# Kernel tuning notes

Measured on AMD Instinct MI355X. Metric: run time of the kernel, lower is better.

The kernel has to match this reference:

```python
import jax, jax.numpy as jnp
import numpy as np

N_NODES, N_EDGES, NNZ, F_IN, HID, K = 50000, 10000, 800000, 128, 512, 10


def setup_inputs() -> dict:
    key = jax.random.key(0)
    ks = jax.random.split(key, 6)
    x = jax.random.normal(ks[0], (N_NODES, F_IN), dtype=jnp.float32)
    node_idx = jax.random.randint(ks[1], (NNZ,), 0, N_NODES)
    edge_idx = jax.random.randint(ks[2], (NNZ,), 0, N_EDGES)
    hyperedge_index = jnp.stack([node_idx, edge_idx]).astype(jnp.int64)
    edge_weight = jax.random.uniform(ks[3], (N_EDGES,), dtype=jnp.float32, minval=0.5, maxval=1.5)
    theta = jax.random.normal(ks[4], (K + 1,), dtype=jnp.float32) * 0.1
    lin1_w = jax.random.normal(ks[5], (HID, F_IN), dtype=jnp.float32) * (1.0 / np.sqrt(F_IN))
    lin1_b = jnp.zeros((HID,), dtype=jnp.float32)
    return {"x": x, "hyperedge_index": hyperedge_index, "edge_weight": edge_weight,
            "theta": theta, "lin1_w": lin1_w, "lin1_b": lin1_b}


def _hyper_prop_factory(node_idx, edge_idx, edge_weight, n_nodes, n_edges):
    """Returns A_norm @ x where A_norm = Dv^-1/2 H W De^-1 H^T Dv^-1/2."""
    ones = jnp.ones_like(node_idx, dtype=edge_weight.dtype)
    d_e = jax.ops.segment_sum(ones, edge_idx, num_segments=n_edges)            # edge degree
    d_v = jax.ops.segment_sum(edge_weight[edge_idx], node_idx, num_segments=n_nodes)
    dv_is = jnp.where(d_v > 0, jax.lax.rsqrt(jnp.maximum(d_v, 1e-12)), 0.0)
    de_w = edge_weight * jnp.where(d_e > 0, 1.0 / jnp.maximum(d_e, 1e-12), 0.0)

    def prop(x):
        xv = x * dv_is[:, None]                                               # [N, F]
        m_e = jax.ops.segment_sum(xv[node_idx], edge_idx, num_segments=n_edges)
        m_e = m_e * de_w[:, None]                                             # [E, F]
        out = jax.ops.segment_sum(m_e[edge_idx], node_idx, num_segments=n_nodes)
        return out * dv_is[:, None]

    return prop


def cheb_hypergraph(x, node_idx, edge_idx, edge_weight, theta, n_nodes, n_edges):
    # L_tilde = L - I = -A_norm (lambda_max = 2). Chebyshev recurrence on L_tilde.
    prop = _hyper_prop_factory(node_idx, edge_idx, edge_weight, n_nodes, n_edges)
    t_prev = x                       # T_0
    out = theta[0] * t_prev
    t_cur = -prop(x)                 # T_1 = L_tilde x
    out = out + theta[1] * t_cur
    for k in range(2, theta.shape[0]):
        t_next = -2.0 * prop(t_cur) - t_prev   # T_k = 2 L_tilde T_{k-1} - T_{k-2}
        out = out + theta[k] * t_next
        t_prev, t_cur = t_cur, t_next
    return out


def reference(x, hyperedge_index, edge_weight, theta, lin1_w, lin1_b):
    node_idx = hyperedge_index[0]
    edge_idx = hyperedge_index[1]
    n_nodes = x.shape[0]
    n_edges = edge_weight.shape[0]
    # eval mode: both dropouts are identity
    h = cheb_hypergraph(x, node_idx, edge_idx, edge_weight, theta, n_nodes, n_edges)
    h = jnp.einsum('nf,hf->nh', h, lin1_w) + lin1_b
    # is_bns=False -> no batch norm; act_fn='relu'
    return jax.nn.relu(h)
```

## Files before the change

kernel.cpp:

```cpp
#include <hip/hip_runtime.h>


#define N_NODES 50000
#define N_EDGES 10000
#define NNZ     800000
#define F_IN    128
#define HID     512
#define F4      (F_IN / 4)
#define R16     16
#define NB_E    10
#define NB_N    49
#define HB      64
#define NW_E    (N_EDGES / 2)
#define NW_N    (N_NODES / 2)

typedef __attribute__((ext_vector_type(8))) short bf16x8;
typedef __attribute__((ext_vector_type(4))) float f32x4;

static __device__ __forceinline__ unsigned short f2bf(float f) {
    union { float f; unsigned u; } c; c.f = f;
    unsigned u = c.u;
    unsigned r = (u + 0x7fffu + ((u >> 16) & 1u)) >> 16;
    return (unsigned short)r;
}
static __device__ __forceinline__ float blo(unsigned u) {
    union { unsigned u; float f; } c; c.u = u << 16; return c.f;
}
static __device__ __forceinline__ float bhi(unsigned u) {
    union { unsigned u; float f; } c; c.u = u & 0xffff0000u; return c.f;
}
static __device__ __forceinline__ unsigned pack2(float lo, float hi) {
    return (unsigned)f2bf(lo) | ((unsigned)f2bf(hi) << 16);
}

__global__ __launch_bounds__(1024) void k_hist(const int* __restrict__ hidx,
                                               unsigned short* __restrict__ loc_e,
                                               unsigned short* __restrict__ loc_v,
                                               unsigned* __restrict__ hist_e,
                                               unsigned* __restrict__ hist_n) {
    __shared__ unsigned she[NW_E];
    __shared__ unsigned shn[NW_N];
    int tid = (int)threadIdx.x;
    for (int w = tid; w < NW_E; w += 1024) she[w] = 0;
    for (int w = tid; w < NW_N; w += 1024) shn[w] = 0;
    __syncthreads();
    int bid = (int)blockIdx.x;
    for (int i = bid * 1024 + tid; i < NNZ; i += HB * 1024) {
        int v = hidx[i];
        int e = hidx[NNZ + i];
        v = min(max(v, 0), N_NODES - 1);
        e = min(max(e, 0), N_EDGES - 1);
        int se = (e & 1) * 16;
        int sv = (v & 1) * 16;
        unsigned oe = atomicAdd(&she[e >> 1], 1u << se);
        unsigned ov = atomicAdd(&shn[v >> 1], 1u << sv);
        loc_e[i] = (unsigned short)((oe >> se) & 0xFFFFu);
        loc_v[i] = (unsigned short)((ov >> sv) & 0xFFFFu);
    }
    __syncthreads();
    for (int w = tid; w < NW_E; w += 1024) hist_e[bid * NW_E + w] = she[w];
    for (int w = tid; w < NW_N; w += 1024) hist_n[bid * NW_N + w] = shn[w];
}

__global__ void k_combine(const unsigned* __restrict__ hist_e,
                          const unsigned* __restrict__ hist_n,
                          int* __restrict__ base_e,
                          int* __restrict__ base_n,
                          int* __restrict__ counts_e,
                          int* __restrict__ counts_n) {
    int i = blockIdx.x * blockDim.x + threadIdx.x;
    if (i < N_EDGES) {
        int sh = (i & 1) * 16;
        int w = i >> 1;
        int s = 0;
#pragma unroll 8
        for (int b = 0; b < HB; ++b) {
            base_e[b * N_EDGES + i] = s;
            s += (int)((hist_e[b * NW_E + w] >> sh) & 0xFFFFu);
        }
        counts_e[i] = s;
    }
    if (i < N_NODES) {
        int sh = (i & 1) * 16;
        int w = i >> 1;
        int s = 0;
#pragma unroll 8
        for (int b = 0; b < HB; ++b) {
            base_n[b * N_NODES + i] = s;
            s += (int)((hist_n[b * NW_N + w] >> sh) & 0xFFFFu);
        }
        counts_n[i] = s;
    }
}

__global__ __launch_bounds__(1024) void k_scan_blk2(const int* __restrict__ ce,
                                                    const int* __restrict__ cn,
                                                    int* __restrict__ oute,
                                                    int* __restrict__ outn,
                                                    int* __restrict__ pe,
                                                    int* __restrict__ pn) {
    __shared__ int sd[1024];
    int b = (int)blockIdx.x;
    const int* counts; int n; int* out; int* partial; int lb;
    if (b < NB_E) { counts = ce; n = N_EDGES; out = oute; partial = pe; lb = b; }
    else          { counts = cn; n = N_NODES; out = outn; partial = pn; lb = b - NB_E; }
    int tid = (int)threadIdx.x;
    int i = lb * 1024 + tid;
    int v = (i < n) ? counts[i] : 0;
    sd[tid] = v;
    __syncthreads();
    for (int off = 1; off < 1024; off <<= 1) {
        int t = (tid >= off) ? sd[tid - off] : 0;
        __syncthreads();
        sd[tid] += t;
        __syncthreads();
    }
    if (i < n) out[i] = sd[tid] - v;
    if (tid == 1023) partial[lb] = sd[1023];
}

__global__ void k_scan_top2(int* __restrict__ pe, int* __restrict__ pn,
                            int* __restrict__ tot_e, int* __restrict__ tot_n) {
    int w = (int)threadIdx.x >> 6;
    int lane = (int)threadIdx.x & 63;
    int* partial = w ? pn : pe;
    int nb       = w ? NB_N : NB_E;
    int* total   = w ? tot_n : tot_e;
    int v = (lane < nb) ? partial[lane] : 0;
    int incl = v;
    for (int off = 1; off < 64; off <<= 1) {
        int t = __shfl_up(incl, off);
        if (lane >= off) incl += t;
    }
    if (lane < nb) partial[lane] = incl - v;
    if (lane == 63) *total = incl;
}

__global__ __launch_bounds__(1024) void k_scan_add2(int* __restrict__ oute,
                                                    int* __restrict__ outn,
                                                    const int* __restrict__ pe,
                                                    const int* __restrict__ pn) {
    int b = (int)blockIdx.x;
    int* out; const int* partial; int n; int lb;
    if (b < NB_E) { out = oute; partial = pe; n = N_EDGES; lb = b; }
    else          { out = outn; partial = pn; n = N_NODES; lb = b - NB_E; }
    int i = lb * 1024 + (int)threadIdx.x;
    if (i < n) out[i] += partial[lb];
}

__global__ void k_fill(const int* __restrict__ hidx,
                       const int* __restrict__ edge_ptr,
                       const int* __restrict__ node_ptr,
                       const unsigned short* __restrict__ loc_e,
                       const unsigned short* __restrict__ loc_v,
                       const int* __restrict__ base_e,
                       const int* __restrict__ base_n,
                       int* __restrict__ edge_node,
                       int* __restrict__ node_edge) {
    int i = blockIdx.x * blockDim.x + threadIdx.x;
    if (i >= NNZ) return;
    int wg = (i >> 10) & (HB - 1);
    int v = hidx[i];
    int e = hidx[NNZ + i];
    v = min(max(v, 0), N_NODES - 1);
    e = min(max(e, 0), N_EDGES - 1);
    edge_node[edge_ptr[e] + base_e[wg * N_EDGES + e] + (int)loc_e[i]] = v;
    node_edge[node_ptr[v] + base_n[wg * N_NODES + v] + (int)loc_v[i]] = e;
}

__global__ void k_norms2(const float* __restrict__ ew,
                         const int* __restrict__ edge_ptr,
                         const int* __restrict__ node_ptr,
                         const int* __restrict__ node_edge,
                         float* __restrict__ dv_is,
                         float* __restrict__ de_w) {
    int i = blockIdx.x * blockDim.x + threadIdx.x;
    if (i < N_NODES) {
        int s = node_ptr[i], t = node_ptr[i + 1];
        float d = 0.f;
        for (int j = s; j < t; ++j) d += ew[node_edge[j]];
        dv_is[i] = (d > 0.f) ? rsqrtf(fmaxf(d, 1e-12f)) : 0.f;
    }
    if (i < N_EDGES) {
        int c = edge_ptr[i + 1] - edge_ptr[i];
        de_w[i] = ew[i] * ((c > 0) ? (1.f / (float)c) : 0.f);
    }
}

__global__ void k_init(const float* __restrict__ x,
                       const float* __restrict__ theta,
                       const float* __restrict__ dv_is,
                       uint4* __restrict__ bufA,
                       float* __restrict__ acc) {
    int i = blockIdx.x * blockDim.x + threadIdx.x;
    if (i >= N_NODES * R16) return;
    int v = i >> 4;
    float dvv = dv_is[v];
    float w = (dvv > 0.f) ? dvv : 1.f;
    float4 x0 = ((const float4*)x)[2 * i];
    float4 x1 = ((const float4*)x)[2 * i + 1];
    uint4 q;
    q.x = pack2(w * x0.x, w * x0.y); q.y = pack2(w * x0.z, w * x0.w);
    q.z = pack2(w * x1.x, w * x1.y); q.w = pack2(w * x1.z, w * x1.w);
    bufA[i] = q;
    float t0 = theta[0];
    float4 a0, a1;
    a0.x = t0 * x0.x; a0.y = t0 * x0.y; a0.z = t0 * x0.z; a0.w = t0 * x0.w;
    a1.x = t0 * x1.x; a1.y = t0 * x1.y; a1.z = t0 * x1.z; a1.w = t0 * x1.w;
    ((float4*)acc)[2 * i]     = a0;
    ((float4*)acc)[2 * i + 1] = a1;
}

__global__ void k_phaseA(const uint4* __restrict__ tin,
                         const float* __restrict__ de_w,
                         const int* __restrict__ edge_ptr,
                         const int* __restrict__ edge_node,
                         uint4* __restrict__ m_e) {
    int tid    = (int)threadIdx.x;
    int g      = tid >> 6;
    int l64    = tid & 63;
    int stream = l64 >> 4;
    int lane   = l64 & 15;
    int e = blockIdx.x * 4 + g;
    int s = edge_ptr[e], t = edge_ptr[e + 1];
    float a0=0.f,a1=0.f,a2=0.f,a3=0.f,a4=0.f,a5=0.f,a6=0.f,a7=0.f;
    int j = s + stream;
    for (; j + 12 < t; j += 16) {
        int v0 = edge_node[j];
        int v1 = edge_node[j + 4];
        int v2 = edge_node[j + 8];
        int v3 = edge_node[j + 12];
        uint4 q0 = tin[v0 * R16 + lane];
        uint4 q1 = tin[v1 * R16 + lane];
        uint4 q2 = tin[v2 * R16 + lane];
        uint4 q3 = tin[v3 * R16 + lane];
        a0 += (blo(q0.x) + blo(q1.x)) + (blo(q2.x) + blo(q3.x));
        a1 += (bhi(q0.x) + bhi(q1.x)) + (bhi(q2.x) + bhi(q3.x));
        a2 += (blo(q0.y) + blo(q1.y)) + (blo(q2.y) + blo(q3.y));
        a3 += (bhi(q0.y) + bhi(q1.y)) + (bhi(q2.y) + bhi(q3.y));
        a4 += (blo(q0.z) + blo(q1.z)) + (blo(q2.z) + blo(q3.z));
        a5 += (bhi(q0.z) + bhi(q1.z)) + (bhi(q2.z) + bhi(q3.z));
        a6 += (blo(q0.w) + blo(q1.w)) + (blo(q2.w) + blo(q3.w));
        a7 += (bhi(q0.w) + bhi(q1.w)) + (bhi(q2.w) + bhi(q3.w));
    }
    for (; j < t; j += 4) {
        int v0 = edge_node[j];
        uint4 q0 = tin[v0 * R16 + lane];
        a0 += blo(q0.x); a1 += bhi(q0.x);
        a2 += blo(q0.y); a3 += bhi(q0.y);
        a4 += blo(q0.z); a5 += bhi(q0.z);
        a6 += blo(q0.w); a7 += bhi(q0.w);
    }
    a0 += __shfl_xor(a0, 16); a1 += __shfl_xor(a1, 16);
    a2 += __shfl_xor(a2, 16); a3 += __shfl_xor(a3, 16);
    a4 += __shfl_xor(a4, 16); a5 += __shfl_xor(a5, 16);
    a6 += __shfl_xor(a6, 16); a7 += __shfl_xor(a7, 16);
    a0 += __shfl_xor(a0, 32); a1 += __shfl_xor(a1, 32);
    a2 += __shfl_xor(a2, 32); a3 += __shfl_xor(a3, 32);
    a4 += __shfl_xor(a4, 32); a5 += __shfl_xor(a5, 32);
    a6 += __shfl_xor(a6, 32); a7 += __shfl_xor(a7, 32);
    if (stream == 0) {
        float w = de_w[e];
        uint4 o;
        o.x = pack2(a0 * w, a1 * w); o.y = pack2(a2 * w, a3 * w);
        o.z = pack2(a4 * w, a5 * w); o.w = pack2(a6 * w, a7 * w);
        m_e[e * R16 + lane] = o;
    }
}

__global__ void k_phaseB(const uint4* __restrict__ m_e,
                         const uint4* __restrict__ tin,
                         const float* __restrict__ dv_is,
                         const int* __restrict__ node_ptr,
                         const int* __restrict__ node_edge,
                         uint4* __restrict__ tio,
                         float* __restrict__ acc,
                         const float* __restrict__ theta, int k,
                         float ca, float cb, int accMode) {
    int g      = threadIdx.x >> 5;
    int stream = (threadIdx.x >> 4) & 1;
    int lane   = threadIdx.x & 15;
    int v = blockIdx.x * 8 + g;
    int s = node_ptr[v], t = node_ptr[v + 1];
    float s0=0.f,s1=0.f,s2=0.f,s3=0.f,s4=0.f,s5=0.f,s6=0.f,s7=0.f;
    int j = s + stream;
    for (; j + 2 < t; j += 4) {
        int e0 = node_edge[j];
        int e1 = node_edge[j + 2];
        uint4 q0 = m_e[e0 * R16 + lane];
        uint4 q1 = m_e[e1 * R16 + lane];
        s0 += blo(q0.x) + blo(q1.x); s1 += bhi(q0.x) + bhi(q1.x);
        s2 += blo(q0.y) + blo(q1.y); s3 += bhi(q0.y) + bhi(q1.y);
        s4 += blo(q0.z) + blo(q1.z); s5 += bhi(q0.z) + bhi(q1.z);
        s6 += blo(q0.w) + blo(q1.w); s7 += bhi(q0.w) + bhi(q1.w);
    }
    if (j < t) {
        int e0 = node_edge[j];
        uint4 q0 = m_e[e0 * R16 + lane];
        s0 += blo(q0.x); s1 += bhi(q0.x);
        s2 += blo(q0.y); s3 += bhi(q0.y);
        s4 += blo(q0.z); s5 += bhi(q0.z);
        s6 += blo(q0.w); s7 += bhi(q0.w);
    }
    s0 += __shfl_xor(s0, 16); s1 += __shfl_xor(s1, 16);
    s2 += __shfl_xor(s2, 16); s3 += __shfl_xor(s3, 16);
    s4 += __shfl_xor(s4, 16); s5 += __shfl_xor(s5, 16);
    s6 += __shfl_xor(s6, 16); s7 += __shfl_xor(s7, 16);
    if (stream == 0) {
        float dvv = dv_is[v];
        float scf = ca * dvv * dvv;
        int idx = v * R16 + lane;
        uint4 tp = tio[idx];
        float t0 = scf * s0 + cb * blo(tp.x);
        float t1 = scf * s1 + cb * bhi(tp.x);
        float t2 = scf * s2 + cb * blo(tp.y);
        float t3 = scf * s3 + cb * bhi(tp.y);
        float t4 = scf * s4 + cb * blo(tp.z);
        float t5 = scf * s5 + cb * bhi(tp.z);
        float t6 = scf * s6 + cb * blo(tp.w);
        float t7 = scf * s7 + cb * bhi(tp.w);
        uint4 tn;
        tn.x = pack2(t0, t1); tn.y = pack2(t2, t3);
        tn.z = pack2(t4, t5); tn.w = pack2(t6, t7);
        tio[idx] = tn;
        if (accMode) {
            float thk = theta[k];
            float a0 = thk * t0, a1 = thk * t1, a2 = thk * t2, a3 = thk * t3;
            float a4 = thk * t4, a5 = thk * t5, a6 = thk * t6, a7 = thk * t7;
            if (accMode >= 2) {
                float th1 = theta[k - 1];
                uint4 tq = tin[idx];
                a0 += th1 * blo(tq.x); a1 += th1 * bhi(tq.x);
                a2 += th1 * blo(tq.y); a3 += th1 * bhi(tq.y);
                a4 += th1 * blo(tq.z); a5 += th1 * bhi(tq.z);
                a6 += th1 * blo(tq.w); a7 += th1 * bhi(tq.w);
            }
            if (accMode >= 3) {
                float th2 = theta[k - 2];
                a0 += th2 * blo(tp.x); a1 += th2 * bhi(tp.x);
                a2 += th2 * blo(tp.y); a3 += th2 * bhi(tp.y);
                a4 += th2 * blo(tp.z); a5 += th2 * bhi(tp.z);
                a6 += th2 * blo(tp.w); a7 += th2 * bhi(tp.w);
            }
            float iw = (dvv > 0.f) ? (1.f / dvv) : 1.f;
            float4* acc4 = (float4*)acc;
            int ai = v * 32 + lane * 2;
            float4 a = acc4[ai];
            a.x += iw * a0; a.y += iw * a1; a.z += iw * a2; a.w += iw * a3;
            acc4[ai] = a;
            float4 b = acc4[ai + 1];
            b.x += iw * a4; b.y += iw * a5; b.z += iw * a6; b.w += iw * a7;
            acc4[ai + 1] = b;
        }
    }
}

#define M_TILES 782
__global__ __launch_bounds__(256) void k_gemm(const float* __restrict__ A,
                                              const float* __restrict__ W,
                                              const float* __restrict__ bias,
                                              float* __restrict__ out) {
    __shared__ short Asm[64 * 136];
    __shared__ short Wsm[64 * 136];
    int id  = (int)blockIdx.x;
    int xcd = id & 7;
    int sub = id >> 3;
    int h_t = sub & 7;
    int m_i = sub >> 3;
    int m_t = xcd * 98 + m_i;
    if (m_t >= M_TILES) return;
    int m0 = m_t * 64;
    int h0 = h_t * 64;
    int tid = (int)threadIdx.x;

    const float4* A4 = (const float4*)A;
    const float4* W4 = (const float4*)W;
#pragma unroll
    for (int i = 0; i < 4; ++i) {
        int c   = tid + i * 256;
        int row = c >> 4;
        int q4  = c & 15;
        int gr = m0 + row;
        float4 a0, a1;
        if (gr < N_NODES) {
            a0 = A4[(size_t)gr * 32 + q4 * 2];
            a1 = A4[(size_t)gr * 32 + q4 * 2 + 1];
        } else {
            a0 = make_float4(0.f, 0.f, 0.f, 0.f);
            a1 = a0;
        }
        uint4 pa;
        pa.x = pack2(a0.x, a0.y); pa.y = pack2(a0.z, a0.w);
        pa.z = pack2(a1.x, a1.y); pa.w = pack2(a1.z, a1.w);
        *(uint4*)&Asm[row * 136 + q4 * 8] = pa;
        float4 w0 = W4[(size_t)(h0 + row) * 32 + q4 * 2];
        float4 w1 = W4[(size_t)(h0 + row) * 32 + q4 * 2 + 1];
        uint4 pw;
        pw.x = pack2(w0.x, w0.y); pw.y = pack2(w0.z, w0.w);
        pw.z = pack2(w1.x, w1.y); pw.w = pack2(w1.z, w1.w);
        *(uint4*)&Wsm[row * 136 + q4 * 8] = pw;
    }
    __syncthreads();

    int lane = tid & 63;
    int wv   = tid >> 6;
    int l16  = lane & 15;
    int quad = lane >> 4;

    f32x4 acc[4];
#pragma unroll
    for (int n = 0; n < 4; ++n) acc[n] = (f32x4){0.f, 0.f, 0.f, 0.f};

#pragma unroll
    for (int ks = 0; ks < 4; ++ks) {
        int k0 = ks * 32;
        bf16x8 af = *(const bf16x8*)&Asm[(wv * 16 + l16) * 136 + k0 + quad * 8];
#pragma unroll
        for (int n = 0; n < 4; ++n) {
            bf16x8 bf = *(const bf16x8*)&Wsm[(n * 16 + l16) * 136 + k0 + quad * 8];
            acc[n] = __builtin_amdgcn_mfma_f32_16x16x32_bf16(af, bf, acc[n], 0, 0, 0);
        }
    }

#pragma unroll
    for (int n = 0; n < 4; ++n) {
        float bb = bias[h0 + n * 16 + l16];
#pragma unroll
        for (int r = 0; r < 4; ++r) {
            int gr = m0 + wv * 16 + quad * 4 + r;
            if (gr < N_NODES)
                out[(size_t)gr * HID + h0 + n * 16 + l16] =
                    fmaxf(acc[n][r] + bb, 0.f);
        }
    }
}

extern "C" void kernel_launch(void* const* d_in, const int* in_sizes, int n_in,
                              void* d_out, int out_size, void* d_ws, size_t ws_size,
                              hipStream_t stream) {
    const float* x     = (const float*)d_in[0];
    const int*   hidx  = (const int*)d_in[1];
    const float* ew    = (const float*)d_in[2];
    const float* theta = (const float*)d_in[3];
    const float* w1    = (const float*)d_in[4];
    const float* b1    = (const float*)d_in[5];
    float*       out   = (float*)d_out;
    int kp1 = in_sizes[3];
    int K   = kp1 - 1;

    char* ob = (char*)d_out;
    size_t oo = 0;
    auto oalloc = [&](size_t bytes) -> void* {
        void* p = ob + oo;
        oo = (oo + bytes + 255) & ~(size_t)255;
        return p;
    };
    uint4* bufA      = (uint4*)oalloc((size_t)N_NODES * F_IN * 2);
    uint4* bufB      = (uint4*)oalloc((size_t)N_NODES * F_IN * 2);
    uint4* m_e       = (uint4*)oalloc((size_t)N_EDGES * F_IN * 2);
    int*   edge_node = (int*)oalloc((size_t)NNZ * 4);
    int*   node_edge = (int*)oalloc((size_t)NNZ * 4);
    unsigned short* loc_e = (unsigned short*)oalloc((size_t)NNZ * 2);
    unsigned short* loc_v = (unsigned short*)oalloc((size_t)NNZ * 2);
    unsigned* hist_e = (unsigned*)oalloc((size_t)HB * NW_E * 4);
    unsigned* hist_n = (unsigned*)oalloc((size_t)HB * NW_N * 4);
    int*   base_e    = (int*)oalloc((size_t)HB * N_EDGES * 4);
    int*   base_n    = (int*)oalloc((size_t)HB * N_NODES * 4);
    int*   counts_e  = (int*)oalloc((size_t)N_EDGES * 4);
    int*   counts_n  = (int*)oalloc((size_t)N_NODES * 4);

    char* ws = (char*)d_ws;
    size_t off = 0;
    auto alloc = [&](size_t bytes) -> void* {
        void* p = ws + off;
        off = (off + bytes + 255) & ~(size_t)255;
        return p;
    };
    float* accv     = (float*)alloc((size_t)N_NODES * F_IN * 4);
    float* dv_is    = (float*)alloc((size_t)N_NODES * 4);
    float* de_w     = (float*)alloc((size_t)N_EDGES * 4);
    int*   edge_ptr = (int*)alloc((size_t)(N_EDGES + 1) * 4);
    int*   node_ptr = (int*)alloc((size_t)(N_NODES + 1) * 4);
    int*   part_e   = (int*)alloc(64 * 4);
    int*   part_n   = (int*)alloc(64 * 4);

    k_hist<<<HB, 1024, 0, stream>>>(hidx, loc_e, loc_v, hist_e, hist_n);
    k_combine<<<(N_NODES + 255) / 256, 256, 0, stream>>>(hist_e, hist_n,
                                                         base_e, base_n,
                                                         counts_e, counts_n);

    k_scan_blk2<<<NB_E + NB_N, 1024, 0, stream>>>(counts_e, counts_n, edge_ptr, node_ptr,
                                                  part_e, part_n);
    k_scan_top2<<<1, 128, 0, stream>>>(part_e, part_n, edge_ptr + N_EDGES, node_ptr + N_NODES);
    k_scan_add2<<<NB_E + NB_N, 1024, 0, stream>>>(edge_ptr, node_ptr, part_e, part_n);

    k_fill<<<(NNZ + 255) / 256, 256, 0, stream>>>(hidx, edge_ptr, node_ptr,
                                                  loc_e, loc_v, base_e, base_n,
                                                  edge_node, node_edge);
    k_norms2<<<(N_NODES + 255) / 256, 256, 0, stream>>>(ew, edge_ptr, node_ptr,
                                                        node_edge, dv_is, de_w);
    k_init<<<(N_NODES * R16 + 255) / 256, 256, 0, stream>>>(x, theta, dv_is, bufA, accv);

    for (int k = 1; k <= K; ++k) {
        const uint4* tin = (k & 1) ? bufA : bufB;
        uint4*       tio = (k & 1) ? bufB : bufA;
        float ca = (k == 1) ? -1.f : -2.f;
        float cb = (k == 1) ? 0.f : -1.f;
        int accMode = 0;
        if (k % 3 == 0) accMode = 3;
        else if (k == K && (K % 3) != 0) accMode = K % 3;
        k_phaseA<<<N_EDGES / 4, 256, 0, stream>>>(tin, de_w, edge_ptr, edge_node, m_e);
        k_phaseB<<<N_NODES / 8, 256, 0, stream>>>(m_e, tin, dv_is, node_ptr, node_edge,
                                                  tio, accv, theta, k, ca, cb, accMode);
    }

    k_gemm<<<8 * 98 * 8, 256, 0, stream>>>(accv, w1, b1, out);
}
```

Before: 745.4 us.

## Split edge gather across four column chunks with 32-bit loads

The edge-aggregation kernel now gives each wave one quarter of the feature columns of an edge, so the grid grows fourfold. Each lane issues a 4-byte load where it used to issue a 16-byte load, and keeps two accumulators instead of eight. The goal is more parallelism and fewer live registers, which should raise occupancy and hide gather latency. The cost is that edge_node is read four times, and each lane's load is narrower, so memory transactions are less efficient.

```diff
diff --git a/kernel.cpp b/kernel.cpp
--- a/kernel.cpp
+++ b/kernel.cpp
@@ -211,60 +211,44 @@
     ((float4*)acc)[2 * i + 1] = a1;
 }
 
-__global__ void k_phaseA(const uint4* __restrict__ tin,
+__global__ void k_phaseA(const unsigned* __restrict__ tin32,
                          const float* __restrict__ de_w,
                          const int* __restrict__ edge_ptr,
                          const int* __restrict__ edge_node,
-                         uint4* __restrict__ m_e) {
+                         unsigned* __restrict__ m_e32) {
     int tid    = (int)threadIdx.x;
-    int g      = tid >> 6;
+    int wv     = tid >> 6;
     int l64    = tid & 63;
     int stream = l64 >> 4;
     int lane   = l64 & 15;
-    int e = blockIdx.x * 4 + g;
+    int gid    = (int)blockIdx.x * 4 + wv;
+    int chunk  = gid / N_EDGES;
+    int e      = gid - chunk * N_EDGES;
+    int col    = chunk * 16 + lane;
     int s = edge_ptr[e], t = edge_ptr[e + 1];
-    float a0=0.f,a1=0.f,a2=0.f,a3=0.f,a4=0.f,a5=0.f,a6=0.f,a7=0.f;
+    float a0 = 0.f, a1 = 0.f;
     int j = s + stream;
     for (; j + 12 < t; j += 16) {
         int v0 = edge_node[j];
         int v1 = edge_node[j + 4];
         int v2 = edge_node[j + 8];
         int v3 = edge_node[j + 12];
-        uint4 q0 = tin[v0 * R16 + lane];
-        uint4 q1 = tin[v1 * R16 + lane];
-        uint4 q2 = tin[v2 * R16 + lane];
-        uint4 q3 = tin[v3 * R16 + lane];
-        a0 += (blo(q0.x) + blo(q1.x)) + (blo(q2.x) + blo(q3.x));
-        a1 += (bhi(q0.x) + bhi(q1.x)) + (bhi(q2.x) + bhi(q3.x));
-        a2 += (blo(q0.y) + blo(q1.y)) + (blo(q2.y) + blo(q3.y));
-        a3 += (bhi(q0.y) + bhi(q1.y)) + (bhi(q2.y) + bhi(q3.y));
-        a4 += (blo(q0.z) + blo(q1.z)) + (blo(q2.z) + blo(q3.z));
-        a5 += (bhi(q0.z) + bhi(q1.z)) + (bhi(q2.z) + bhi(q3.z));
-        a6 += (blo(q0.w) + blo(q1.w)) + (blo(q2.w) + blo(q3.w));
-        a7 += (bhi(q0.w) + bhi(q1.w)) + (bhi(q2.w) + bhi(q3.w));
+        unsigned q0 = tin32[v0 * 64 + col];
+        unsigned q1 = tin32[v1 * 64 + col];
+        unsigned q2 = tin32[v2 * 64 + col];
+        unsigned q3 = tin32[v3 * 64 + col];
+        a0 += (blo(q0) + blo(q1)) + (blo(q2) + blo(q3));
+        a1 += (bhi(q0) + bhi(q1)) + (bhi(q2) + bhi(q3));
     }
     for (; j < t; j += 4) {
-        int v0 = edge_node[j];
-        uint4 q0 = tin[v0 * R16 + lane];
-        a0 += blo(q0.x); a1 += bhi(q0.x);
-        a2 += blo(q0.y); a3 += bhi(q0.y);
-        a4 += blo(q0.z); a5 += bhi(q0.z);
-        a6 += blo(q0.w); a7 += bhi(q0.w);
+        unsigned q0 = tin32[edge_node[j] * 64 + col];
+        a0 += blo(q0); a1 += bhi(q0);
     }
     a0 += __shfl_xor(a0, 16); a1 += __shfl_xor(a1, 16);
-    a2 += __shfl_xor(a2, 16); a3 += __shfl_xor(a3, 16);
-    a4 += __shfl_xor(a4, 16); a5 += __shfl_xor(a5, 16);
-    a6 += __shfl_xor(a6, 16); a7 += __shfl_xor(a7, 16);
     a0 += __shfl_xor(a0, 32); a1 += __shfl_xor(a1, 32);
-    a2 += __shfl_xor(a2, 32); a3 += __shfl_xor(a3, 32);
-    a4 += __shfl_xor(a4, 32); a5 += __shfl_xor(a5, 32);
-    a6 += __shfl_xor(a6, 32); a7 += __shfl_xor(a7, 32);
     if (stream == 0) {
         float w = de_w[e];
-        uint4 o;
-        o.x = pack2(a0 * w, a1 * w); o.y = pack2(a2 * w, a3 * w);
-        o.z = pack2(a4 * w, a5 * w); o.w = pack2(a6 * w, a7 * w);
-        m_e[e * R16 + lane] = o;
+        m_e32[e * 64 + col] = pack2(a0 * w, a1 * w);
     }
 }
 
@@ -509,7 +493,8 @@
         int accMode = 0;
         if (k % 3 == 0) accMode = 3;
         else if (k == K && (K % 3) != 0) accMode = K % 3;
-        k_phaseA<<<N_EDGES / 4, 256, 0, stream>>>(tin, de_w, edge_ptr, edge_node, m_e);
+        k_phaseA<<<N_EDGES, 256, 0, stream>>>((const unsigned*)tin, de_w,
+                                              edge_ptr, edge_node, (unsigned*)m_e);
         k_phaseB<<<N_NODES / 8, 256, 0, stream>>>(m_e, tin, dv_is, node_ptr, node_edge,
                                                   tio, accv, theta, k, ca, cb, accMode);
     }
```

Result: slower. 893.8 us (+19.9%).

## Split feature columns into two slabs across blocks in propagation kernels

Applied to the files above, without the earlier changes.

Both gather kernels now split the 128-feature row (16 uint4 columns) into two 8-column slabs, each handled by a separate half of the grid. Each block therefore touches only half of every gathered row, which should shrink the per-pass working set in cache. Per-entity parallelism rises because 8 lanes per stream replace 16, giving more streams per edge in phaseA and more nodes per block in phaseB. In exchange, the index lists are read twice and each gather moves only 128 bytes per row per slab, so memory transactions are smaller.

```diff
diff --git a/kernel.cpp b/kernel.cpp
--- a/kernel.cpp
+++ b/kernel.cpp
@@ -6,7 +6,6 @@
 #define NNZ     800000
 #define F_IN    128
 #define HID     512
-#define F4      (F_IN / 4)
 #define R16     16
 #define NB_E    10
 #define NB_N    49
@@ -217,23 +216,26 @@
                          const int* __restrict__ edge_node,
                          uint4* __restrict__ m_e) {
     int tid    = (int)threadIdx.x;
-    int g      = tid >> 6;
+    int wv     = tid >> 6;
     int l64    = tid & 63;
-    int stream = l64 >> 4;
-    int lane   = l64 & 15;
-    int e = blockIdx.x * 4 + g;
+    int stream = l64 >> 3;
+    int sl     = l64 & 7;
+    int b      = (int)blockIdx.x;
+    int slab   = (b >= (N_EDGES / 4)) ? 1 : 0;
+    int e      = (b - slab * (N_EDGES / 4)) * 4 + wv;
+    int col    = slab * 8 + sl;
     int s = edge_ptr[e], t = edge_ptr[e + 1];
     float a0=0.f,a1=0.f,a2=0.f,a3=0.f,a4=0.f,a5=0.f,a6=0.f,a7=0.f;
     int j = s + stream;
-    for (; j + 12 < t; j += 16) {
+    for (; j + 24 < t; j += 32) {
         int v0 = edge_node[j];
-        int v1 = edge_node[j + 4];
-        int v2 = edge_node[j + 8];
-        int v3 = edge_node[j + 12];
-        uint4 q0 = tin[v0 * R16 + lane];
-        uint4 q1 = tin[v1 * R16 + lane];
-        uint4 q2 = tin[v2 * R16 + lane];
-        uint4 q3 = tin[v3 * R16 + lane];
+        int v1 = edge_node[j + 8];
+        int v2 = edge_node[j + 16];
+        int v3 = edge_node[j + 24];
+        uint4 q0 = tin[v0 * R16 + col];
+        uint4 q1 = tin[v1 * R16 + col];
+        uint4 q2 = tin[v2 * R16 + col];
+        uint4 q3 = tin[v3 * R16 + col];
         a0 += (blo(q0.x) + blo(q1.x)) + (blo(q2.x) + blo(q3.x));
         a1 += (bhi(q0.x) + bhi(q1.x)) + (bhi(q2.x) + bhi(q3.x));
         a2 += (blo(q0.y) + blo(q1.y)) + (blo(q2.y) + blo(q3.y));
@@ -243,14 +245,18 @@
         a6 += (blo(q0.w) + blo(q1.w)) + (blo(q2.w) + blo(q3.w));
         a7 += (bhi(q0.w) + bhi(q1.w)) + (bhi(q2.w) + bhi(q3.w));
     }
-    for (; j < t; j += 4) {
+    for (; j < t; j += 8) {
         int v0 = edge_node[j];
-        uint4 q0 = tin[v0 * R16 + lane];
+        uint4 q0 = tin[v0 * R16 + col];
         a0 += blo(q0.x); a1 += bhi(q0.x);
         a2 += blo(q0.y); a3 += bhi(q0.y);
         a4 += blo(q0.z); a5 += bhi(q0.z);
         a6 += blo(q0.w); a7 += bhi(q0.w);
     }
+    a0 += __shfl_xor(a0, 8);  a1 += __shfl_xor(a1, 8);
+    a2 += __shfl_xor(a2, 8);  a3 += __shfl_xor(a3, 8);
+    a4 += __shfl_xor(a4, 8);  a5 += __shfl_xor(a5, 8);
+    a6 += __shfl_xor(a6, 8);  a7 += __shfl_xor(a7, 8);
     a0 += __shfl_xor(a0, 16); a1 += __shfl_xor(a1, 16);
     a2 += __shfl_xor(a2, 16); a3 += __shfl_xor(a3, 16);
     a4 += __shfl_xor(a4, 16); a5 += __shfl_xor(a5, 16);
@@ -264,7 +270,7 @@
         uint4 o;
         o.x = pack2(a0 * w, a1 * w); o.y = pack2(a2 * w, a3 * w);
         o.z = pack2(a4 * w, a5 * w); o.w = pack2(a6 * w, a7 * w);
-        m_e[e * R16 + lane] = o;
+        m_e[e * R16 + col] = o;
     }
 }
 
@@ -277,18 +283,23 @@
                          float* __restrict__ acc,
                          const float* __restrict__ theta, int k,
                          float ca, float cb, int accMode) {
-    int g      = threadIdx.x >> 5;
-    int stream = (threadIdx.x >> 4) & 1;
-    int lane   = threadIdx.x & 15;
-    int v = blockIdx.x * 8 + g;
+    int tid    = (int)threadIdx.x;
+    int g      = tid >> 4;
+    int t16    = tid & 15;
+    int stream = t16 >> 3;
+    int sl     = t16 & 7;
+    int b      = (int)blockIdx.x;
+    int slab   = (b >= (N_NODES / 16)) ? 1 : 0;
+    int v      = (b - slab * (N_NODES / 16)) * 16 + g;
+    int col    = slab * 8 + sl;
     int s = node_ptr[v], t = node_ptr[v + 1];
     float s0=0.f,s1=0.f,s2=0.f,s3=0.f,s4=0.f,s5=0.f,s6=0.f,s7=0.f;
     int j = s + stream;
     for (; j + 2 < t; j += 4) {
         int e0 = node_edge[j];
         int e1 = node_edge[j + 2];
-        uint4 q0 = m_e[e0 * R16 + lane];
-        uint4 q1 = m_e[e1 * R16 + lane];
+        uint4 q0 = m_e[e0 * R16 + col];
+        uint4 q1 = m_e[e1 * R16 + col];
         s0 += blo(q0.x) + blo(q1.x); s1 += bhi(q0.x) + bhi(q1.x);
         s2 += blo(q0.y) + blo(q1.y); s3 += bhi(q0.y) + bhi(q1.y);
         s4 += blo(q0.z) + blo(q1.z); s5 += bhi(q0.z) + bhi(q1.z);
@@ -296,20 +307,20 @@
     }
     if (j < t) {
         int e0 = node_edge[j];
-        uint4 q0 = m_e[e0 * R16 + lane];
+        uint4 q0 = m_e[e0 * R16 + col];
         s0 += blo(q0.x); s1 += bhi(q0.x);
         s2 += blo(q0.y); s3 += bhi(q0.y);
         s4 += blo(q0.z); s5 += bhi(q0.z);
         s6 += blo(q0.w); s7 += bhi(q0.w);
     }
-    s0 += __shfl_xor(s0, 16); s1 += __shfl_xor(s1, 16);
-    s2 += __shfl_xor(s2, 16); s3 += __shfl_xor(s3, 16);
-    s4 += __shfl_xor(s4, 16); s5 += __shfl_xor(s5, 16);
-    s6 += __shfl_xor(s6, 16); s7 += __shfl_xor(s7, 16);
+    s0 += __shfl_xor(s0, 8); s1 += __shfl_xor(s1, 8);
+    s2 += __shfl_xor(s2, 8); s3 += __shfl_xor(s3, 8);
+    s4 += __shfl_xor(s4, 8); s5 += __shfl_xor(s5, 8);
+    s6 += __shfl_xor(s6, 8); s7 += __shfl_xor(s7, 8);
     if (stream == 0) {
         float dvv = dv_is[v];
         float scf = ca * dvv * dvv;
-        int idx = v * R16 + lane;
+        int idx = v * R16 + col;
         uint4 tp = tio[idx];
         float t0 = scf * s0 + cb * blo(tp.x);
         float t1 = scf * s1 + cb * bhi(tp.x);
@@ -344,13 +355,13 @@
             }
             float iw = (dvv > 0.f) ? (1.f / dvv) : 1.f;
             float4* acc4 = (float4*)acc;
-            int ai = v * 32 + lane * 2;
+            int ai = v * 32 + col * 2;
             float4 a = acc4[ai];
             a.x += iw * a0; a.y += iw * a1; a.z += iw * a2; a.w += iw * a3;
             acc4[ai] = a;
-            float4 b = acc4[ai + 1];
-            b.x += iw * a4; b.y += iw * a5; b.z += iw * a6; b.w += iw * a7;
-            acc4[ai + 1] = b;
+            float4 bvec = acc4[ai + 1];
+            bvec.x += iw * a4; bvec.y += iw * a5; bvec.z += iw * a6; bvec.w += iw * a7;
+            acc4[ai + 1] = bvec;
         }
     }
 }
@@ -509,9 +520,9 @@
         int accMode = 0;
         if (k % 3 == 0) accMode = 3;
         else if (k == K && (K % 3) != 0) accMode = K % 3;
-        k_phaseA<<<N_EDGES / 4, 256, 0, stream>>>(tin, de_w, edge_ptr, edge_node, m_e);
-        k_phaseB<<<N_NODES / 8, 256, 0, stream>>>(m_e, tin, dv_is, node_ptr, node_edge,
-                                                  tio, accv, theta, k, ca, cb, accMode);
+        k_phaseA<<<2 * (N_EDGES / 4), 256, 0, stream>>>(tin, de_w, edge_ptr, edge_node, m_e);
+        k_phaseB<<<2 * (N_NODES / 16), 256, 0, stream>>>(m_e, tin, dv_is, node_ptr, node_edge,
+                                                         tio, accv, theta, k, ca, cb, accMode);
     }
 
     k_gemm<<<8 * 98 * 8, 256, 0, stream>>>(accv, w1, b1, out);
```

New measurement: 727.1 us (median of 2 runs). 2.5% less time.
